# Kernel optimization log

Hardware: AMD Instinct MI355X
Metric: run time of the kernel (lower is better)

The kernel has to match this reference:

```python
import jax, jax.numpy as jnp
import numpy as np

BN_EPS = 1e-5


def setup_inputs() -> dict:
    key = jax.random.key(0)
    ks = jax.random.split(key, 12)
    B, N, S, D1, D2 = 8, 8192, 2048, 128, 256
    C_in = D2 + D1  # 384
    mlp = [256, 128]
    inp = {
        "xyz1": jax.random.normal(ks[0], (B, 3, N), jnp.float32),
        "xyz2": jax.random.normal(ks[1], (B, 3, S), jnp.float32),
        "points1": jax.random.normal(ks[2], (B, D1, N), jnp.float32),
        "points2": jax.random.normal(ks[3], (B, D2, S), jnp.float32),
    }
    # conv0: in 384 -> 256, conv1: 256 -> 128 (1x1 Conv1d == per-point matmul)
    inp["w0"] = jax.random.normal(ks[4], (mlp[0], C_in), jnp.float32) * (1.0 / np.sqrt(C_in))
    inp["b0"] = jax.random.normal(ks[5], (mlp[0],), jnp.float32) * 0.01
    inp["g0"] = jnp.ones((mlp[0],), jnp.float32)
    inp["be0"] = jnp.zeros((mlp[0],), jnp.float32)
    inp["w1"] = jax.random.normal(ks[6], (mlp[1], mlp[0]), jnp.float32) * (1.0 / np.sqrt(mlp[0]))
    inp["b1"] = jax.random.normal(ks[7], (mlp[1],), jnp.float32) * 0.01
    inp["g1"] = jnp.ones((mlp[1],), jnp.float32)
    inp["be1"] = jnp.zeros((mlp[1],), jnp.float32)
    return inp


def _conv_bn_relu(x, w, b, g, be):
    # 1x1 Conv1d + BatchNorm1d (training-mode batch stats, biased var) + ReLU
    x = jnp.einsum("oc,bcn->bon", w, x) + b[None, :, None]
    m = jnp.mean(x, axis=(0, 2), keepdims=True)
    v = jnp.var(x, axis=(0, 2), keepdims=True)
    x = (x - m) * jax.lax.rsqrt(v + BN_EPS) * g[None, :, None] + be[None, :, None]
    return jax.nn.relu(x)


def reference(xyz1, xyz2, points1, points2, w0, b0, g0, be0, w1, b1, g1, be1):
    B, _, N = xyz1.shape
    S = xyz2.shape[2]
    src = jnp.transpose(xyz1, (0, 2, 1))  # [B,N,3]
    dst = jnp.transpose(xyz2, (0, 2, 1))  # [B,S,3]
    # squared pairwise distance [B,N,S]
    dist = (
        jnp.sum(src * src, axis=-1)[:, :, None]
        + jnp.sum(dst * dst, axis=-1)[:, None, :]
        - 2.0 * jnp.einsum("bnc,bsc->bns", src, dst)
    )
    # 3 nearest neighbors (smallest dist, sorted)
    neg_d, idx = jax.lax.top_k(-dist, 3)  # [B,N,3]
    d3 = -neg_d
    recip = 1.0 / (d3 + 1e-8)
    weight = recip / jnp.sum(recip, axis=-1, keepdims=True)  # [B,N,3]
    p2t = jnp.transpose(points2, (0, 2, 1))  # [B,S,D']
    gathered = jnp.take_along_axis(
        p2t, idx.reshape(B, N * 3)[:, :, None], axis=1
    ).reshape(B, N, 3, -1)  # [B,N,3,D']
    interp = jnp.einsum("bnkd,bnk->bdn", gathered, weight)  # [B,D',N]
    x = jnp.concatenate([interp, points1], axis=1)  # [B,D'+D,N]
    x = _conv_bn_relu(x, w0, b0, g0, be0)
    x = _conv_bn_relu(x, w1, b1, g1, be1)
    return x
```

## Files before the change

kernel.cpp:

```cpp
#include <hip/hip_runtime.h>
#include <hip/hip_bf16.h>

constexpr int kB = 8, kN = 8192, kS = 2048;
constexpr int kD1 = 128, kD2 = 256, kCin = 384, kM0 = 256, kM1 = 128;
constexpr float kEps = 1e-5f;
constexpr int kReps = 64;

typedef float f32x4 __attribute__((ext_vector_type(4)));
typedef short bf16x8 __attribute__((ext_vector_type(8)));
typedef unsigned short u16x4 __attribute__((ext_vector_type(4)));

__device__ inline unsigned short f2bf(float f) {
    __hip_bfloat16 h = __float2bfloat16(f);
    return *reinterpret_cast<unsigned short*>(&h);
}
__device__ inline float bf2f(unsigned short u) {
    unsigned int v = (unsigned int)u << 16;
    return *reinterpret_cast<float*>(&v);
}
__device__ inline unsigned uminu(unsigned a, unsigned b) { return a < b ? a : b; }
__device__ inline unsigned med3u(unsigned a, unsigned b, unsigned c) {
    unsigned d;
    asm("v_med3_u32 %0, %1, %2, %3" : "=v"(d) : "v"(a), "v"(b), "v"(c));
    return d;
}
#define INS4(K0, K1, K2, K3, X) do { unsigned _x = (X);          \
    K3 = med3u(_x, K2, K3);                                      \
    K2 = med3u(_x, K1, K2);                                      \
    K1 = med3u(_x, K0, K1);                                      \
    K0 = uminu(_x, K0); } while (0)

__global__ __launch_bounds__(256) void prep_kernel(
    const float* __restrict__ points2, float* __restrict__ p2t,
    const float* __restrict__ points1, unsigned short* __restrict__ xt,
    const float* __restrict__ xyz2, f32x4* __restrict__ spk,
    float* __restrict__ repl, float* __restrict__ smallstats,
    const float* __restrict__ w0, unsigned short* __restrict__ w0bf,
    const float* __restrict__ w1, unsigned short* __restrict__ w1bf)
{
    __shared__ float tl[64][69];
    const int bx = blockIdx.x;
    const int t = threadIdx.x;
    const int rlo = t >> 4, rhi = t & 15;
    if (bx < 1024) {
        const int b = bx >> 7, tile = bx & 127;
        const int s0 = (tile & 31) * 64, c0 = (tile >> 5) * 64;
#pragma unroll
        for (int r = 0; r < 4; ++r) {
            const int cl = rlo + r * 16;
            f32x4 v = *(const f32x4*)(points2 + ((size_t)(b * kD2 + c0 + cl)) * kS + s0 + rhi * 4);
#pragma unroll
            for (int j = 0; j < 4; ++j) tl[cl][rhi * 4 + j] = v[j];
        }
        __syncthreads();
#pragma unroll
        for (int r = 0; r < 4; ++r) {
            const int sl = rlo + r * 16;
            f32x4 v;
#pragma unroll
            for (int j = 0; j < 4; ++j) v[j] = tl[rhi * 4 + j][sl];
            *(f32x4*)(p2t + ((size_t)(b * kS + s0 + sl)) * kD2 + c0 + rhi * 4) = v;
        }
    } else if (bx < 3072) {
        const int idx = bx - 1024;
        const int b = idx >> 8, tile = idx & 255;
        const int n0 = (tile & 127) * 64, c0 = (tile >> 7) * 64;
#pragma unroll
        for (int r = 0; r < 4; ++r) {
            const int cl = rlo + r * 16;
            f32x4 v = *(const f32x4*)(points1 + ((size_t)(b * kD1 + c0 + cl)) * kN + n0 + rhi * 4);
#pragma unroll
            for (int j = 0; j < 4; ++j) tl[cl][rhi * 4 + j] = v[j];
        }
        __syncthreads();
#pragma unroll
        for (int r = 0; r < 4; ++r) {
            const int nl = rlo + r * 16;
            u16x4 u;
#pragma unroll
            for (int j = 0; j < 4; ++j) u[j] = f2bf(tl[rhi * 4 + j][nl]);
            *(u16x4*)(xt + ((size_t)(b * kN + n0 + nl)) * kCin + 256 + c0 + rhi * 4) = u;
        }
    } else if (bx < 3080) {
        const int b = bx - 3072;
        const float* x2 = xyz2 + b * 3 * kS;
        for (int s = t; s < kS; s += 256) {
            float sx = x2[s], sy = x2[kS + s], sz = x2[2 * kS + s];
            f32x4 q = {sx, sy, sz, fmaf(sx, sx, fmaf(sy, sy, sz * sz))};
            spk[b * kS + s] = q;
        }
        for (int i = b * 6144 + t; i < (b + 1) * 6144; i += 256) repl[i] = 0.f;
        if (b == 0) for (int i = t; i < 772; i += 256) smallstats[i] = 0.f;
    } else if (bx < 3096) {
        const int base = (bx - 3080) * 256 + t;
        for (int c = base; c < kM0 * kCin / 4; c += 4096) {
            f32x4 v = *(const f32x4*)(w0 + (size_t)c * 4);
            u16x4 u = {f2bf(v[0]), f2bf(v[1]), f2bf(v[2]), f2bf(v[3])};
            *(u16x4*)(w0bf + (size_t)c * 4) = u;
        }
    } else {
        const int base = (bx - 3096) * 256 + t;
        for (int c = base; c < kM1 * kM0 / 4; c += 2048) {
            f32x4 v = *(const f32x4*)(w1 + (size_t)c * 4);
            u16x4 u = {f2bf(v[0]), f2bf(v[1]), f2bf(v[2]), f2bf(v[3])};
            *(u16x4*)(w1bf + (size_t)c * 4) = u;
        }
    }
}

__global__ __launch_bounds__(256) void knn_interp_kernel(
    const float* __restrict__ xyz1, const f32x4* __restrict__ spk,
    const float* __restrict__ p2t, unsigned short* __restrict__ xt,
    int* __restrict__ flaglist, int* __restrict__ flagcount)
{
    __shared__ f32x4 sp[kS];
    __shared__ float gw[64][3];
    __shared__ int   gi[64][3];
    const int bb = blockIdx.x >> 7;
    const int nblk = (blockIdx.x & 127) << 6;
    const int t = threadIdx.x;
    for (int s = t; s < kS; s += 256) sp[s] = spk[bb * kS + s];
    __syncthreads();
    const int grp = t >> 4, l16 = t & 15;
    const int q0 = nblk + grp * 4;
    const float* x1 = xyz1 + bb * 3 * kN;
    float ax[4], ay[4], az[4], ppv[4];
#pragma unroll
    for (int j = 0; j < 4; ++j) {
        const float px = x1[q0 + j], py = x1[kN + q0 + j], pz = x1[2 * kN + q0 + j];
        ax[j] = -2.f * px; ay[j] = -2.f * py; az[j] = -2.f * pz;
        ppv[j] = fmaf(px, px, fmaf(py, py, pz * pz));
    }

    unsigned ka[4], kb[4], kc[4], kd[4];
#pragma unroll
    for (int j = 0; j < 4; ++j) { ka[j] = kb[j] = kc[j] = kd[j] = 0xFFFFFFFFu; }
#pragma unroll 4
    for (int i = 0; i < 128; ++i) {
        const int s = l16 + 16 * i;
        const f32x4 qv = sp[s];
#pragma unroll
        for (int j = 0; j < 4; ++j) {
            const float e = fmaxf(fmaf(ax[j], qv[0], fmaf(ay[j], qv[1],
                                fmaf(az[j], qv[2], qv[3] + ppv[j]))), 0.f);
            const unsigned x = (__float_as_uint(e) & 0xFFFFF800u) | (unsigned)s;
            INS4(ka[j], kb[j], kc[j], kd[j], x);
        }
    }
#pragma unroll
    for (int off = 1; off <= 8; off <<= 1) {
#pragma unroll
        for (int j = 0; j < 4; ++j) {
            const unsigned m0 = __shfl_xor(ka[j], off), m1 = __shfl_xor(kb[j], off);
            const unsigned m2 = __shfl_xor(kc[j], off), m3 = __shfl_xor(kd[j], off);
            INS4(ka[j], kb[j], kc[j], kd[j], m0); INS4(ka[j], kb[j], kc[j], kd[j], m1);
            INS4(ka[j], kb[j], kc[j], kd[j], m2); INS4(ka[j], kb[j], kc[j], kd[j], m3);
        }
    }

    bool flag = false;
    if (l16 < 4) {
        const unsigned c0 = l16 == 0 ? ka[0] : l16 == 1 ? ka[1] : l16 == 2 ? ka[2] : ka[3];
        const unsigned c1 = l16 == 0 ? kb[0] : l16 == 1 ? kb[1] : l16 == 2 ? kb[2] : kb[3];
        const unsigned c2 = l16 == 0 ? kc[0] : l16 == 1 ? kc[1] : l16 == 2 ? kc[2] : kc[3];
        const unsigned c3 = l16 == 0 ? kd[0] : l16 == 1 ? kd[1] : l16 == 2 ? kd[2] : kd[3];
        const float axx = l16 == 0 ? ax[0] : l16 == 1 ? ax[1] : l16 == 2 ? ax[2] : ax[3];
        const float ayy = l16 == 0 ? ay[0] : l16 == 1 ? ay[1] : l16 == 2 ? ay[2] : ay[3];
        const float azz = l16 == 0 ? az[0] : l16 == 1 ? az[1] : l16 == 2 ? az[2] : az[3];
        int i0 = (int)(c0 & 2047u), i1 = (int)(c1 & 2047u), i2 = (int)(c2 & 2047u);
        const float v2t = __uint_as_float(c2 & 0xFFFFF800u);
        const float v3t = __uint_as_float(c3 & 0xFFFFF800u);
        flag = (v3t - v2t) <= fmaf(v3t, 1e-3f, 2.5e-4f);
        const double dpx = -0.5 * (double)axx, dpy = -0.5 * (double)ayy, dpz = -0.5 * (double)azz;
        const f32x4 s0 = sp[i0], s1 = sp[i1], s2 = sp[i2];
        double d0 = (dpx - s0[0]) * (dpx - s0[0]) + (dpy - s0[1]) * (dpy - s0[1]) + (dpz - s0[2]) * (dpz - s0[2]);
        double d1 = (dpx - s1[0]) * (dpx - s1[0]) + (dpy - s1[1]) * (dpy - s1[1]) + (dpz - s1[2]) * (dpz - s1[2]);
        double d2 = (dpx - s2[0]) * (dpx - s2[0]) + (dpy - s2[1]) * (dpy - s2[1]) + (dpz - s2[2]) * (dpz - s2[2]);
        if (d1 < d0 || (d1 == d0 && i1 < i0)) { double td = d0; d0 = d1; d1 = td; int ti = i0; i0 = i1; i1 = ti; }
        if (d2 < d1 || (d2 == d1 && i2 < i1)) { double td = d1; d1 = d2; d2 = td; int ti = i1; i1 = i2; i2 = ti; }
        if (d1 < d0 || (d1 == d0 && i1 < i0)) { double td = d0; d0 = d1; d1 = td; int ti = i0; i0 = i1; i1 = ti; }
        const double r0 = 1.0 / (d0 + 1e-8), r1 = 1.0 / (d1 + 1e-8), r2 = 1.0 / (d2 + 1e-8);
        const double rs = 1.0 / (r0 + r1 + r2);
        const int gq = grp * 4 + l16;
        gw[gq][0] = (float)(r0 * rs); gw[gq][1] = (float)(r1 * rs); gw[gq][2] = (float)(r2 * rs);
        gi[gq][0] = i0; gi[gq][1] = i1; gi[gq][2] = i2;
    }
    {
        const unsigned long long bal = __ballot(flag);
        if (bal) {
            const int l = t & 63;
            int base = 0;
            if (l == 0) base = atomicAdd(flagcount, __popcll(bal));
            base = __shfl(base, 0);
            if (flag) {
                const int pre = __popcll(bal & ((1ull << l) - 1ull));
                flaglist[base + pre] = (bb << 13) | (nblk + grp * 4 + l16);
            }
        }
    }
    __syncthreads();

    const int q = t >> 2, c4 = t & 3;
    const int nq = nblk + q;
    const float w0f = gw[q][0], w1f = gw[q][1], w2f = gw[q][2];
    const f32x4* row0 = (const f32x4*)(p2t + ((size_t)(bb * kS) + gi[q][0]) * kD2);
    const f32x4* row1 = (const f32x4*)(p2t + ((size_t)(bb * kS) + gi[q][1]) * kD2);
    const f32x4* row2 = (const f32x4*)(p2t + ((size_t)(bb * kS) + gi[q][2]) * kD2);
    unsigned short* dst = xt + ((size_t)(bb * kN) + nq) * kCin;
#pragma unroll 4
    for (int j = 0; j < 16; ++j) {
        const int ch = c4 + 4 * j;
        f32x4 v = w0f * row0[ch] + w1f * row1[ch] + w2f * row2[ch];
        u16x4 u = {f2bf(v[0]), f2bf(v[1]), f2bf(v[2]), f2bf(v[3])};
        *(u16x4*)(dst + ch * 4) = u;
    }
}
#undef INS4

__global__ __launch_bounds__(256) void knn_fallback_kernel(
    const float* __restrict__ xyz1, const f32x4* __restrict__ spk,
    const float* __restrict__ p2t, unsigned short* __restrict__ xt,
    const int* __restrict__ flaglist, const int* __restrict__ flagcount)
{
    const int cnt = *flagcount;
    const int t = threadIdx.x;
    const int w = t >> 6, l = t & 63;
    for (int idx = blockIdx.x * 4 + w; idx < cnt; idx += gridDim.x * 4) {
        const int code = flaglist[idx];
        const int b = code >> 13, n = code & 8191;
        const float* x1 = xyz1 + b * 3 * kN;
        const double px = (double)x1[n], py = (double)x1[kN + n], pz = (double)x1[2 * kN + n];
        double d0 = 1e300, d1 = 1e300, d2 = 1e300;
        int i0 = 0, i1 = 0, i2 = 0;
        for (int s = l; s < kS; s += 64) {
            const f32x4 q = spk[b * kS + s];
            const double ex = px - (double)q[0], ey = py - (double)q[1], ez = pz - (double)q[2];
            const double d = ex * ex + ey * ey + ez * ez;
            if (d < d2) {
                if (d < d1) {
                    if (d < d0) { d2 = d1; i2 = i1; d1 = d0; i1 = i0; d0 = d; i0 = s; }
                    else        { d2 = d1; i2 = i1; d1 = d;  i1 = s; }
                } else          { d2 = d;  i2 = s; }
            }
        }
#pragma unroll
        for (int off = 1; off < 64; off <<= 1) {
            double pd0 = __shfl_xor(d0, off), pd1 = __shfl_xor(d1, off), pd2 = __shfl_xor(d2, off);
            int pi0 = __shfl_xor(i0, off), pi1 = __shfl_xor(i1, off), pi2 = __shfl_xor(i2, off);
#pragma unroll
            for (int m = 0; m < 3; ++m) {
                const double pd = (m == 0) ? pd0 : (m == 1) ? pd1 : pd2;
                const int pi = (m == 0) ? pi0 : (m == 1) ? pi1 : pi2;
                if (pd < d2 || (pd == d2 && pi < i2)) {
                    if (pd < d1 || (pd == d1 && pi < i1)) {
                        if (pd < d0 || (pd == d0 && pi < i0)) {
                            d2 = d1; i2 = i1; d1 = d0; i1 = i0; d0 = pd; i0 = pi;
                        } else { d2 = d1; i2 = i1; d1 = pd; i1 = pi; }
                    } else { d2 = pd; i2 = pi; }
                }
            }
        }
        const double r0 = 1.0 / (d0 + 1e-8), r1 = 1.0 / (d1 + 1e-8), r2 = 1.0 / (d2 + 1e-8);
        const double rs = 1.0 / (r0 + r1 + r2);
        const float w0f = (float)(r0 * rs), w1f = (float)(r1 * rs), w2f = (float)(r2 * rs);
        const f32x4* row0 = (const f32x4*)(p2t + ((size_t)(b * kS) + i0) * kD2);
        const f32x4* row1 = (const f32x4*)(p2t + ((size_t)(b * kS) + i1) * kD2);
        const f32x4* row2 = (const f32x4*)(p2t + ((size_t)(b * kS) + i2) * kD2);
        const f32x4 v = w0f * row0[l] + w1f * row1[l] + w2f * row2[l];
        u16x4 u = {f2bf(v[0]), f2bf(v[1]), f2bf(v[2]), f2bf(v[3])};
        *(u16x4*)(xt + ((size_t)(b * kN) + n) * kCin + l * 4) = u;
    }
}

__device__ inline int swz(int row, int ks) {
    return row * 32 + ((ks ^ ((row >> 1) & 3)) << 3);
}

template <int K, int MTOT, bool BNRELU, int OUTMODE, bool STATS>
__global__ __launch_bounds__(256) void gemm_bn_kernel(
    const unsigned short* __restrict__ Wbf, const unsigned short* __restrict__ X,
    const float* __restrict__ scale, const float* __restrict__ shift,
    unsigned short* __restrict__ Yb, float* __restrict__ Yf,
    float* __restrict__ repl)
{
    constexpr int BM = 128, BN = 64;
    __shared__ unsigned short Al[2][BM * 32], Bl[2][BN * 32];
    __shared__ float ssum[BM], ssq[BM];
    __shared__ float s_sc[K], s_sh[K];
    const int t = threadIdx.x;
    const int bn = blockIdx.x * BN, bo = blockIdx.y * BM, b = blockIdx.z;
    const int l = t & 63, w = t >> 6;
    const int wm = (w >> 1) * 64, wn = (w & 1) * 32;
    const int lrow = l & 15, lks = l >> 4;

    if constexpr (BNRELU) {
        if (t < K) { s_sc[t] = scale[t]; s_sh[t] = shift[t]; }
    }
    if constexpr (STATS) {
        if (t < BM) { ssum[t] = 0.f; ssq[t] = 0.f; }
    }
    __syncthreads();

    const int mA0 = t >> 2, ksA = t & 3;
    const int mA1 = mA0 + 64;
    const int nB = t >> 2, ksB = t & 3;
    bf16x8 rA0, rA1, rB;

    auto load_tile = [&](int k0) {
        rA0 = *(const bf16x8*)(Wbf + (size_t)(bo + mA0) * K + k0 + ksA * 8);
        rA1 = *(const bf16x8*)(Wbf + (size_t)(bo + mA1) * K + k0 + ksA * 8);
        rB  = *(const bf16x8*)(X + ((size_t)(b * kN) + bn + nB) * K + k0 + ksB * 8);
    };
    auto write_tile = [&](int buf, int k0) {
        *(bf16x8*)(&Al[buf][0] + swz(mA0, ksA)) = rA0;
        *(bf16x8*)(&Al[buf][0] + swz(mA1, ksA)) = rA1;
        bf16x8 v = rB;
        if constexpr (BNRELU) {
#pragma unroll
            for (int j = 0; j < 8; ++j) {
                const int ch = k0 + ksB * 8 + j;
                float f = fmaxf(fmaf(bf2f((unsigned short)v[j]), s_sc[ch], s_sh[ch]), 0.f);
                v[j] = (short)f2bf(f);
            }
        }
        *(bf16x8*)(&Bl[buf][0] + swz(nB, ksB)) = v;
    };

    f32x4 acc[4][2] = {};
    load_tile(0);
    write_tile(0, 0);
    __syncthreads();
    int cur = 0;
    for (int k0 = 32; k0 <= K; k0 += 32) {
        if (k0 < K) load_tile(k0);
        bf16x8 af[4], bfr[2];
#pragma unroll
        for (int f = 0; f < 4; ++f) af[f]  = *(const bf16x8*)(&Al[cur][0] + swz(wm + f * 16 + lrow, lks));
#pragma unroll
        for (int f = 0; f < 2; ++f) bfr[f] = *(const bf16x8*)(&Bl[cur][0] + swz(wn + f * 16 + lrow, lks));
#pragma unroll
        for (int mi = 0; mi < 4; ++mi)
#pragma unroll
            for (int ni = 0; ni < 2; ++ni)
                acc[mi][ni] = __builtin_amdgcn_mfma_f32_16x16x32_bf16(af[mi], bfr[ni], acc[mi][ni], 0, 0, 0);
        if (k0 < K) { write_tile(cur ^ 1, k0); cur ^= 1; }
        __syncthreads();
    }

    if constexpr (STATS) {
#pragma unroll
        for (int mi = 0; mi < 4; ++mi) {
#pragma unroll
            for (int r = 0; r < 4; ++r) {
                float ps = 0.f, pq = 0.f;
#pragma unroll
                for (int ni = 0; ni < 2; ++ni) { float v = acc[mi][ni][r]; ps += v; pq += v * v; }
#pragma unroll
                for (int off = 1; off < 16; off <<= 1) { ps += __shfl_xor(ps, off); pq += __shfl_xor(pq, off); }
                if (lrow == 0) {
                    const int m = wm + mi * 16 + lks * 4 + r;
                    atomicAdd(&ssum[m], ps); atomicAdd(&ssq[m], pq);
                }
            }
        }
    }

    if constexpr (OUTMODE == 0) {
#pragma unroll
        for (int mi = 0; mi < 4; ++mi)
#pragma unroll
            for (int ni = 0; ni < 2; ++ni) {
                const int m = bo + wm + mi * 16 + lks * 4;
                const int n = bn + wn + ni * 16 + lrow;
                u16x4 u = {f2bf(acc[mi][ni][0]), f2bf(acc[mi][ni][1]),
                           f2bf(acc[mi][ni][2]), f2bf(acc[mi][ni][3])};
                *(u16x4*)(Yb + ((size_t)(b * kN) + n) * MTOT + m) = u;
            }
    } else {
#pragma unroll
        for (int mi = 0; mi < 4; ++mi)
#pragma unroll
            for (int ni = 0; ni < 2; ++ni) {
                const int n = bn + wn + ni * 16 + lrow;
#pragma unroll
                for (int r = 0; r < 4; ++r) {
                    const int m = bo + wm + mi * 16 + lks * 4 + r;
                    Yf[((size_t)(b * MTOT) + m) * kN + n] = acc[mi][ni][r];
                }
            }
    }
    if constexpr (STATS) {
        __syncthreads();
        if (t < BM) {
            const int rep = (blockIdx.x + blockIdx.z * 8) & (kReps - 1);
            float* rp = repl + (size_t)rep * (2 * MTOT);
            atomicAdd(&rp[bo + t], ssum[t]);
            atomicAdd(&rp[MTOT + bo + t], ssq[t]);
        }
    }
}

__global__ void bn_finalize_kernel(const float* __restrict__ repl,
                                   const float* __restrict__ g, const float* __restrict__ be,
                                   float* __restrict__ scale, float* __restrict__ shift, int M)
{
    const int t = threadIdx.x;
    if (t < M) {
        float s = 0.f, q = 0.f;
#pragma unroll 8
        for (int r = 0; r < kReps; ++r) {
            s += repl[(size_t)r * 2 * M + t];
            q += repl[(size_t)r * 2 * M + M + t];
        }
        const float invn = 1.0f / 65536.0f;
        const float mean = s * invn;
        const float var = q * invn - mean * mean;
        const float sc = g[t] * rsqrtf(var + kEps);
        scale[t] = sc;
        shift[t] = fmaf(-mean, sc, be[t]);
    }
}

__global__ __launch_bounds__(256) void bn_relu_out_kernel(
    float* __restrict__ out, const float* __restrict__ scale, const float* __restrict__ shift)
{
    const int total = kB * kM1 * kN / 4;
    for (int idx = blockIdx.x * blockDim.x + threadIdx.x; idx < total;
         idx += gridDim.x * blockDim.x) {
        const int p = (idx >> 11) & 127;
        const float sc = scale[p], sh = shift[p];
        f32x4 v = ((f32x4*)out)[idx];
#pragma unroll
        for (int j = 0; j < 4; ++j) v[j] = fmaxf(fmaf(v[j], sc, sh), 0.f);
        ((f32x4*)out)[idx] = v;
    }
}

extern "C" void kernel_launch(void* const* d_in, const int* in_sizes, int n_in,
                              void* d_out, int out_size, void* d_ws, size_t ws_size,
                              hipStream_t stream)
{
    const float* xyz1    = (const float*)d_in[0];
    const float* xyz2    = (const float*)d_in[1];
    const float* points1 = (const float*)d_in[2];
    const float* points2 = (const float*)d_in[3];
    const float* w0      = (const float*)d_in[4];
    const float* g0      = (const float*)d_in[6];
    const float* be0     = (const float*)d_in[7];
    const float* w1      = (const float*)d_in[8];
    const float* g1      = (const float*)d_in[10];
    const float* be1     = (const float*)d_in[11];
    float* out = (float*)d_out;

    char* ws = (char*)d_ws;
    unsigned short* xt  = (unsigned short*)ws;
    float* p2t          = (float*)(ws + (size_t)50331648);
    unsigned short* y0t = (unsigned short*)(ws + (size_t)67108864);
    float* repl0        = (float*)(ws + (size_t)100663296);
    float* repl1        = (float*)(ws + (size_t)100794368);
    float* smallstats   = (float*)(ws + (size_t)100859904);
    f32x4* spk          = (f32x4*)(ws + (size_t)104857600);
    int*  flaglist      = (int*)(ws + (size_t)105906176);
    unsigned short* w0bf = (unsigned short*)(ws + (size_t)106954752);
    unsigned short* w1bf = (unsigned short*)(ws + (size_t)107151360);
    float* scale0 = smallstats,       *shift0 = smallstats + 256;
    float* scale1 = smallstats + 512, *shift1 = smallstats + 640;
    int*  flagcount = (int*)(smallstats + 768);

    prep_kernel<<<3104, 256, 0, stream>>>(points2, p2t, points1, xt, xyz2, spk,
                                          repl0, smallstats, w0, w0bf, w1, w1bf);
    knn_interp_kernel<<<1024, 256, 0, stream>>>(xyz1, spk, p2t, xt, flaglist, flagcount);
    knn_fallback_kernel<<<1024, 256, 0, stream>>>(xyz1, spk, p2t, xt, flaglist, flagcount);
    gemm_bn_kernel<kCin, kM0, false, 0, true><<<dim3(128, 2, 8), 256, 0, stream>>>(
        w0bf, xt, nullptr, nullptr, y0t, nullptr, repl0);
    bn_finalize_kernel<<<1, 256, 0, stream>>>(repl0, g0, be0, scale0, shift0, 256);
    gemm_bn_kernel<kM0, kM1, true, 1, true><<<dim3(128, 1, 8), 256, 0, stream>>>(
        w1bf, y0t, scale0, shift0, nullptr, out, repl1);
    bn_finalize_kernel<<<1, 128, 0, stream>>>(repl1, g1, be1, scale1, shift1, 128);
    bn_relu_out_kernel<<<2048, 256, 0, stream>>>(out, scale1, shift1);
}
```

Measured before the change: 162.0 us.

## Prefilter kNN candidates with float pass and skip sorted inserts above cutoff

Adds a cheap first pass that computes per-query top-3 minimum distances using two min-accumulators per lane, merged across the 16-lane group, to obtain a third-smallest cutoff. The second pass still computes every distance but runs the 4-slot packed-key insertion only when some lane in the wavefront has a candidate at or below the cutoff. This trades a second full distance sweep for skipping most sorted-insertion work, adding a wave-level branch. The per-lane pairwise top-3 approximation may produce a cutoff that is too loose, but it should never be too tight.

Measured after the change: 168.3 us. +3.9%, slower.

```diff
diff --git a/kernel.cpp b/kernel.cpp
--- a/kernel.cpp
+++ b/kernel.cpp
@@ -132,19 +132,65 @@
         ppv[j] = fmaf(px, px, fmaf(py, py, pz * pz));
     }
 
+    float cA[4], cB[4];
+#pragma unroll
+    for (int j = 0; j < 4; ++j) { cA[j] = 1e30f; cB[j] = 1e30f; }
+#pragma unroll 2
+    for (int i = 0; i < 128; i += 2) {
+        const f32x4 qv0 = sp[l16 + 16 * i];
+        const f32x4 qv1 = sp[l16 + 16 * (i + 1)];
+#pragma unroll
+        for (int j = 0; j < 4; ++j) {
+            const float e0 = fmaxf(fmaf(ax[j], qv0[0], fmaf(ay[j], qv0[1],
+                                 fmaf(az[j], qv0[2], qv0[3] + ppv[j]))), 0.f);
+            const float e1 = fmaxf(fmaf(ax[j], qv1[0], fmaf(ay[j], qv1[1],
+                                 fmaf(az[j], qv1[2], qv1[3] + ppv[j]))), 0.f);
+            cA[j] = fminf(cA[j], e0);
+            cB[j] = fminf(cB[j], e1);
+        }
+    }
+    float b0[4], b1[4], b2[4];
+#pragma unroll
+    for (int j = 0; j < 4; ++j) {
+        b0[j] = fminf(cA[j], cB[j]); b1[j] = fmaxf(cA[j], cB[j]); b2[j] = 1e30f;
+    }
+#pragma unroll
+    for (int off = 1; off <= 8; off <<= 1) {
+#pragma unroll
+        for (int j = 0; j < 4; ++j) {
+            const float y0 = __shfl_xor(b0[j], off), y1 = __shfl_xor(b1[j], off), y2 = __shfl_xor(b2[j], off);
+            const float z0 = fminf(b0[j], y0);
+            const float z1 = fminf(fmaxf(b0[j], y0), fminf(b1[j], y1));
+            const float z2 = fminf(fminf(fmaxf(b1[j], y0), fmaxf(b0[j], y1)), fminf(b2[j], y2));
+            b0[j] = z0; b1[j] = z1; b2[j] = z2;
+        }
+    }
+    float cut[4];
+#pragma unroll
+    for (int j = 0; j < 4; ++j) cut[j] = b2[j] + 1e-3f;
+
     unsigned ka[4], kb[4], kc[4], kd[4];
 #pragma unroll
     for (int j = 0; j < 4; ++j) { ka[j] = kb[j] = kc[j] = kd[j] = 0xFFFFFFFFu; }
-#pragma unroll 4
+#pragma unroll 2
     for (int i = 0; i < 128; ++i) {
         const int s = l16 + 16 * i;
         const f32x4 qv = sp[s];
+        float e[4]; int cnd[4];
 #pragma unroll
         for (int j = 0; j < 4; ++j) {
-            const float e = fmaxf(fmaf(ax[j], qv[0], fmaf(ay[j], qv[1],
-                                fmaf(az[j], qv[2], qv[3] + ppv[j]))), 0.f);
-            const unsigned x = (__float_as_uint(e) & 0xFFFFF800u) | (unsigned)s;
-            INS4(ka[j], kb[j], kc[j], kd[j], x);
+            e[j] = fmaxf(fmaf(ax[j], qv[0], fmaf(ay[j], qv[1],
+                        fmaf(az[j], qv[2], qv[3] + ppv[j]))), 0.f);
+            cnd[j] = e[j] <= cut[j];
+        }
+        if (__any(cnd[0] | cnd[1] | cnd[2] | cnd[3])) {
+#pragma unroll
+            for (int j = 0; j < 4; ++j) {
+                const unsigned x = cnd[j]
+                    ? ((__float_as_uint(e[j]) & 0xFFFFF800u) | (unsigned)s)
+                    : 0xFFFFFFFFu;
+                INS4(ka[j], kb[j], kc[j], kd[j], x);
+            }
         }
     }
 #pragma unroll
```
